# Optimization experiments

Measured on AMD Instinct MI355X. Metric: run time of the kernel, lower is better.

The kernel has to match this reference:

```python
import jax, jax.numpy as jnp
import numpy as np

NUM_SEGMENTS = 16


def setup_inputs() -> dict:
    key = jax.random.key(0)
    k1, k2 = jax.random.split(key)
    B, L, H = 8, 4096, 1024
    hidden_states = jax.random.normal(k1, (B, L, H), dtype=jnp.float32)
    # left-aligned variable-length attention mask (torch code assumes left alignment)
    lengths = jax.random.randint(k2, (B,), 1, L + 1)
    attention_mask = (jnp.arange(L)[None, :] < lengths[:, None]).astype(jnp.int32)
    return {"hidden_states": hidden_states, "attention_mask": attention_mask}


def reference(hidden_states, attention_mask):
    """Vectorized equivalent of SegmentPooler.forward.

    Per batch element b:
      valid_len = sum(mask[b])
      boundaries = linspace(0, valid_len, S+1).long()  (endpoint exact)
      segment s pools mean of tokens [start, end) with end clamped to
      min(start+1, valid_len) when end <= start; segments with
      start >= valid_len stay zero and seg_mask False.
    Implemented with a prefix-sum so all (b, s) segment means come from a
    single cumsum pass (segment_reduce style, no Python loops).
    """
    B, L, H = hidden_states.shape
    S = NUM_SEGMENTS
    valid_len = attention_mask.sum(axis=1).astype(jnp.int32)  # [B]

    # torch.linspace(0, valid_len, S+1).long(): float grid truncated toward zero,
    # with the endpoint set exactly to valid_len.
    frac = jnp.arange(S + 1, dtype=jnp.float32) / jnp.float32(S)  # [S+1]
    bounds = jnp.floor(frac[None, :] * valid_len[:, None].astype(jnp.float32)).astype(jnp.int32)
    bounds = bounds.at[:, -1].set(valid_len)  # [B, S+1]

    start = bounds[:, :S]  # [B, S]
    end = bounds[:, 1:]    # [B, S]
    seg_mask = start < valid_len[:, None]  # segments past valid_len stay empty (the `break`)
    end = jnp.where(end <= start, jnp.minimum(start + 1, valid_len[:, None]), end)

    # inclusive prefix sums over tokens, with a leading zero row: [B, L+1, H]
    csum = jnp.concatenate(
        [jnp.zeros((B, 1, H), hidden_states.dtype), jnp.cumsum(hidden_states, axis=1)],
        axis=1,
    )
    sums = (jnp.take_along_axis(csum, end[:, :, None], axis=1)
            - jnp.take_along_axis(csum, start[:, :, None], axis=1))  # [B, S, H]
    count = jnp.maximum(end - start, 1).astype(hidden_states.dtype)  # [B, S]
    seg_states = jnp.where(seg_mask[:, :, None], sums / count[:, :, None], 0.0)
    return seg_states, seg_mask
```

## Files before the change

### kernel.cpp

```cpp
#include <hip/hip_runtime.h>

#define NSEG 16
#define SLICES 8

__global__ void k_prep(const int* __restrict__ mask, int L,
                       int* __restrict__ vlen, float* __restrict__ mout) {
    int b = blockIdx.x;
    const int* m = mask + (size_t)b * L;
    int t = threadIdx.x;
    int s = 0;
    for (int i = t; i < L; i += 256) s += m[i];
    #pragma unroll
    for (int off = 32; off > 0; off >>= 1) s += __shfl_down(s, off, 64);
    __shared__ int sh[4];
    int w = t >> 6;
    if ((t & 63) == 0) sh[w] = s;
    __syncthreads();
    __shared__ int vsh;
    if (t == 0) { int v = sh[0] + sh[1] + sh[2] + sh[3]; vsh = v; vlen[b] = v; }
    __syncthreads();
    if (t < NSEG) {
        int st = (t * vsh) >> 4;
        mout[b * NSEG + t] = (st < vsh) ? 1.0f : 0.0f;
    }
}

__global__ void k_part(const float* __restrict__ x, const int* __restrict__ vlen,
                       float* __restrict__ part, int L, int H) {
    int id = blockIdx.x;
    int sl = id & (SLICES - 1);
    int bs = id / SLICES;
    int b = bs >> 4, s = bs & 15;
    int vl = vlen[b];
    int start = (s * vl) >> 4;
    int end = ((s + 1) * vl) >> 4;
    int n = (start < vl) ? max(end - start, 1) : 0;
    int i0 = (sl * n) / SLICES;
    int i1 = ((sl + 1) * n) / SLICES;
    int cnt = i1 - i0;

    int hbase = blockIdx.y * 256;
    int lane = threadIdx.x;
    const float4* px = (const float4*)(x + ((size_t)b * L + start + i0) * H + hbase) + lane;
    int stride4 = H >> 2;

    float4 a0 = {0,0,0,0}, a1 = {0,0,0,0}, a2 = {0,0,0,0}, a3 = {0,0,0,0};
    int t = 0;
    for (; t + 4 <= cnt; t += 4) {
        float4 v0 = px[0 * stride4];
        float4 v1 = px[1 * stride4];
        float4 v2 = px[2 * stride4];
        float4 v3 = px[3 * stride4];
        px += 4 * stride4;
        a0.x += v0.x; a0.y += v0.y; a0.z += v0.z; a0.w += v0.w;
        a1.x += v1.x; a1.y += v1.y; a1.z += v1.z; a1.w += v1.w;
        a2.x += v2.x; a2.y += v2.y; a2.z += v2.z; a2.w += v2.w;
        a3.x += v3.x; a3.y += v3.y; a3.z += v3.z; a3.w += v3.w;
    }
    for (; t < cnt; ++t) {
        float4 v0 = *px; px += stride4;
        a0.x += v0.x; a0.y += v0.y; a0.z += v0.z; a0.w += v0.w;
    }
    float4 acc;
    acc.x = (a0.x + a1.x) + (a2.x + a3.x);
    acc.y = (a0.y + a1.y) + (a2.y + a3.y);
    acc.z = (a0.z + a1.z) + (a2.z + a3.z);
    acc.w = (a0.w + a1.w) + (a2.w + a3.w);

    float4* pp = (float4*)(part + (size_t)id * H + hbase) + lane;
    *pp = acc;
}

__global__ void k_reduce(const float* __restrict__ part, const int* __restrict__ vlen,
                         float* __restrict__ out, int H) {
    int bs = blockIdx.x;
    int b = bs >> 4, s = bs & 15;
    int vl = vlen[b];
    int start = (s * vl) >> 4;
    int end = ((s + 1) * vl) >> 4;
    int cnt = max(end - start, 1);

    int hbase = blockIdx.y * 256;
    int lane = threadIdx.x;

    float4 acc = {0,0,0,0};
    #pragma unroll
    for (int sl = 0; sl < SLICES; ++sl) {
        const float4* pp = (const float4*)(part + ((size_t)bs * SLICES + sl) * H + hbase) + lane;
        float4 v = *pp;
        acc.x += v.x; acc.y += v.y; acc.z += v.z; acc.w += v.w;
    }
    float scl = 1.0f / (float)cnt;
    acc.x *= scl; acc.y *= scl; acc.z *= scl; acc.w *= scl;

    float4* po = (float4*)(out + (size_t)bs * H + hbase) + lane;
    *po = acc;
}

extern "C" void kernel_launch(void* const* d_in, const int* in_sizes, int n_in,
                              void* d_out, int out_size, void* d_ws, size_t ws_size,
                              hipStream_t stream) {
    const float* hs  = (const float*)d_in[0];
    const int* mask  = (const int*)d_in[1];
    int H = in_sizes[0] / in_sizes[1];
    int B = out_size / (NSEG * (H + 1));
    int L = in_sizes[1] / B;

    float* seg_out  = (float*)d_out;
    float* mask_out = seg_out + (size_t)B * NSEG * H;
    int* vlen = (int*)d_ws;
    float* part = (float*)d_ws + 64;

    k_prep<<<B, 256, 0, stream>>>(mask, L, vlen, mask_out);
    dim3 gridA(B * NSEG * SLICES, H / 256);
    k_part<<<gridA, 64, 0, stream>>>(hs, vlen, part, L, H);
    dim3 gridB(B * NSEG, H / 256);
    k_reduce<<<gridB, 64, 0, stream>>>(part, vlen, seg_out, H);
}
```

Baseline: 23.37 us.

## Fuse mask length reduction into partial-sum kernel and widen blocks to full H

Removes the separate prep kernel: every partial-sum block now recomputes the valid length from the mask with int4 loads, and slice 0 writes vlen and the segment mask. Blocks now span the whole hidden dimension (H/4 threads) instead of 256-column tiles over a 2D grid, and the token loop unrolls by 8 instead of 4. This drops one launch and its dependency gap, but each of the 1024 blocks rereads the 16KB mask row, which adds redundant memory traffic and a block-wide sync before the main loads.

```diff
diff --git a/kernel.cpp b/kernel.cpp
--- a/kernel.cpp
+++ b/kernel.cpp
@@ -3,72 +3,82 @@
 #define NSEG 16
 #define SLICES 8
 
-__global__ void k_prep(const int* __restrict__ mask, int L,
-                       int* __restrict__ vlen, float* __restrict__ mout) {
-    int b = blockIdx.x;
-    const int* m = mask + (size_t)b * L;
-    int t = threadIdx.x;
-    int s = 0;
-    for (int i = t; i < L; i += 256) s += m[i];
-    #pragma unroll
-    for (int off = 32; off > 0; off >>= 1) s += __shfl_down(s, off, 64);
-    __shared__ int sh[4];
-    int w = t >> 6;
-    if ((t & 63) == 0) sh[w] = s;
-    __syncthreads();
-    __shared__ int vsh;
-    if (t == 0) { int v = sh[0] + sh[1] + sh[2] + sh[3]; vsh = v; vlen[b] = v; }
-    __syncthreads();
-    if (t < NSEG) {
-        int st = (t * vsh) >> 4;
-        mout[b * NSEG + t] = (st < vsh) ? 1.0f : 0.0f;
-    }
-}
-
-__global__ void k_part(const float* __restrict__ x, const int* __restrict__ vlen,
-                       float* __restrict__ part, int L, int H) {
+__global__ void k_part(const float* __restrict__ x, const int* __restrict__ mask,
+                       float* __restrict__ part, int* __restrict__ vlen,
+                       float* __restrict__ mout, int L, int H) {
     int id = blockIdx.x;
     int sl = id & (SLICES - 1);
     int bs = id / SLICES;
     int b = bs >> 4, s = bs & 15;
-    int vl = vlen[b];
+    int t = threadIdx.x;
+
+    const int4* m4 = (const int4*)(mask + (size_t)b * L);
+    int n4 = L >> 2;
+    int acc = 0;
+    for (int i = t; i < n4; i += blockDim.x) {
+        int4 v = m4[i];
+        acc += v.x + v.y + v.z + v.w;
+    }
+    #pragma unroll
+    for (int off = 32; off > 0; off >>= 1) acc += __shfl_down(acc, off, 64);
+    __shared__ int sh[8];
+    if ((t & 63) == 0) sh[t >> 6] = acc;
+    __syncthreads();
+    __shared__ int vsh;
+    if (t == 0) {
+        int nw = blockDim.x >> 6;
+        int v = 0;
+        for (int w = 0; w < nw; ++w) v += sh[w];
+        vsh = v;
+        if (sl == 0) {
+            vlen[b] = v;
+            int st = (s * v) >> 4;
+            mout[bs] = (st < v) ? 1.0f : 0.0f;
+        }
+    }
+    __syncthreads();
+    int vl = vsh;
+
     int start = (s * vl) >> 4;
-    int end = ((s + 1) * vl) >> 4;
+    int end   = ((s + 1) * vl) >> 4;
     int n = (start < vl) ? max(end - start, 1) : 0;
     int i0 = (sl * n) / SLICES;
     int i1 = ((sl + 1) * n) / SLICES;
     int cnt = i1 - i0;
 
-    int hbase = blockIdx.y * 256;
-    int lane = threadIdx.x;
-    const float4* px = (const float4*)(x + ((size_t)b * L + start + i0) * H + hbase) + lane;
-    int stride4 = H >> 2;
-
+    const float* base = x + ((size_t)b * L + start + i0) * H + t * 4;
     float4 a0 = {0,0,0,0}, a1 = {0,0,0,0}, a2 = {0,0,0,0}, a3 = {0,0,0,0};
-    int t = 0;
-    for (; t + 4 <= cnt; t += 4) {
-        float4 v0 = px[0 * stride4];
-        float4 v1 = px[1 * stride4];
-        float4 v2 = px[2 * stride4];
-        float4 v3 = px[3 * stride4];
-        px += 4 * stride4;
+    float4 a4 = {0,0,0,0}, a5 = {0,0,0,0}, a6 = {0,0,0,0}, a7 = {0,0,0,0};
+    int r = 0;
+    for (; r + 8 <= cnt; r += 8) {
+        float4 v0 = *(const float4*)(base + (size_t)(r + 0) * H);
+        float4 v1 = *(const float4*)(base + (size_t)(r + 1) * H);
+        float4 v2 = *(const float4*)(base + (size_t)(r + 2) * H);
+        float4 v3 = *(const float4*)(base + (size_t)(r + 3) * H);
+        float4 v4 = *(const float4*)(base + (size_t)(r + 4) * H);
+        float4 v5 = *(const float4*)(base + (size_t)(r + 5) * H);
+        float4 v6 = *(const float4*)(base + (size_t)(r + 6) * H);
+        float4 v7 = *(const float4*)(base + (size_t)(r + 7) * H);
         a0.x += v0.x; a0.y += v0.y; a0.z += v0.z; a0.w += v0.w;
         a1.x += v1.x; a1.y += v1.y; a1.z += v1.z; a1.w += v1.w;
         a2.x += v2.x; a2.y += v2.y; a2.z += v2.z; a2.w += v2.w;
         a3.x += v3.x; a3.y += v3.y; a3.z += v3.z; a3.w += v3.w;
+        a4.x += v4.x; a4.y += v4.y; a4.z += v4.z; a4.w += v4.w;
+        a5.x += v5.x; a5.y += v5.y; a5.z += v5.z; a5.w += v5.w;
+        a6.x += v6.x; a6.y += v6.y; a6.z += v6.z; a6.w += v6.w;
+        a7.x += v7.x; a7.y += v7.y; a7.z += v7.z; a7.w += v7.w;
     }
-    for (; t < cnt; ++t) {
-        float4 v0 = *px; px += stride4;
+    for (; r < cnt; ++r) {
+        float4 v0 = *(const float4*)(base + (size_t)r * H);
         a0.x += v0.x; a0.y += v0.y; a0.z += v0.z; a0.w += v0.w;
     }
-    float4 acc;
-    acc.x = (a0.x + a1.x) + (a2.x + a3.x);
-    acc.y = (a0.y + a1.y) + (a2.y + a3.y);
-    acc.z = (a0.z + a1.z) + (a2.z + a3.z);
-    acc.w = (a0.w + a1.w) + (a2.w + a3.w);
+    float4 out4;
+    out4.x = ((a0.x + a1.x) + (a2.x + a3.x)) + ((a4.x + a5.x) + (a6.x + a7.x));
+    out4.y = ((a0.y + a1.y) + (a2.y + a3.y)) + ((a4.y + a5.y) + (a6.y + a7.y));
+    out4.z = ((a0.z + a1.z) + (a2.z + a3.z)) + ((a4.z + a5.z) + (a6.z + a7.z));
+    out4.w = ((a0.w + a1.w) + (a2.w + a3.w)) + ((a4.w + a5.w) + (a6.w + a7.w));
 
-    float4* pp = (float4*)(part + (size_t)id * H + hbase) + lane;
-    *pp = acc;
+    *(float4*)(part + (size_t)id * H + t * 4) = out4;
 }
 
 __global__ void k_reduce(const float* __restrict__ part, const int* __restrict__ vlen,
@@ -77,24 +87,19 @@
     int b = bs >> 4, s = bs & 15;
     int vl = vlen[b];
     int start = (s * vl) >> 4;
-    int end = ((s + 1) * vl) >> 4;
+    int end   = ((s + 1) * vl) >> 4;
     int cnt = max(end - start, 1);
-
-    int hbase = blockIdx.y * 256;
-    int lane = threadIdx.x;
+    int t = threadIdx.x;
 
     float4 acc = {0,0,0,0};
     #pragma unroll
     for (int sl = 0; sl < SLICES; ++sl) {
-        const float4* pp = (const float4*)(part + ((size_t)bs * SLICES + sl) * H + hbase) + lane;
-        float4 v = *pp;
+        float4 v = *(const float4*)(part + ((size_t)bs * SLICES + sl) * H + t * 4);
         acc.x += v.x; acc.y += v.y; acc.z += v.z; acc.w += v.w;
     }
     float scl = 1.0f / (float)cnt;
     acc.x *= scl; acc.y *= scl; acc.z *= scl; acc.w *= scl;
-
-    float4* po = (float4*)(out + (size_t)bs * H + hbase) + lane;
-    *po = acc;
+    *(float4*)(out + (size_t)bs * H + t * 4) = acc;
 }
 
 extern "C" void kernel_launch(void* const* d_in, const int* in_sizes, int n_in,
@@ -111,9 +116,6 @@
     int* vlen = (int*)d_ws;
     float* part = (float*)d_ws + 64;
 
-    k_prep<<<B, 256, 0, stream>>>(mask, L, vlen, mask_out);
-    dim3 gridA(B * NSEG * SLICES, H / 256);
-    k_part<<<gridA, 64, 0, stream>>>(hs, vlen, part, L, H);
-    dim3 gridB(B * NSEG, H / 256);
-    k_reduce<<<gridB, 64, 0, stream>>>(part, vlen, seg_out, H);
+    k_part<<<B * NSEG * SLICES, H / 4, 0, stream>>>(hs, mask, part, vlen, mask_out, L, H);
+    k_reduce<<<B * NSEG, H / 4, 0, stream>>>(part, vlen, seg_out, H);
 }
```

Result: faster. 20.11 us (-14.0%).
